# Optimization experiments

Hardware: AMD Instinct MI355X
Metric: run time of the kernel (lower is better)

## Reference

```python
import jax, jax.numpy as jnp
import numpy as np

N_FFT = 512
HOP = 128
WIN = 512
LENGTH = 600  # hardcoded in the original forward


def _hann(n):
    # torch.hann_window default is periodic: 0.5*(1-cos(2*pi*i/n))
    i = jnp.arange(n, dtype=jnp.float32)
    return 0.5 * (1.0 - jnp.cos(2.0 * jnp.pi * i / n))


def setup_inputs() -> dict:
    key = jax.random.key(0)
    x = jax.random.normal(key, (8192, 1, 257, 6, 2), dtype=jnp.float32)
    return {"x": x}


def reference(x):
    B, C, F, T, D = x.shape  # C==1, F==n_fft//2+1, D==2
    # view(B, F, T, D) + view_as_complex
    spec = x[:, 0, :, :, 0] + 1j * x[:, 0, :, :, 1]          # [B, F, T] complex64
    # inverse real FFT per frame (torch.istft, normalized=False, onesided=True)
    frames = jnp.fft.irfft(spec.transpose(0, 2, 1), n=N_FFT, axis=-1)  # [B, T, n_fft]
    win = _hann(WIN)                                          # [n_fft] (win_length == n_fft)
    frames = frames * win                                     # synthesis windowing
    # overlap-add
    L = HOP * (T - 1) + N_FFT
    idx = jnp.arange(T)[:, None] * HOP + jnp.arange(N_FFT)[None, :]  # [T, n_fft]
    y = jnp.zeros((B, L), dtype=frames.dtype).at[:, idx].add(frames)  # [B, L]
    # window-square envelope normalization (COLA division)
    env = jnp.zeros((L,), dtype=frames.dtype).at[idx].add(win * win)  # [L]
    # center=True trim of n_fft//2, then length=600 crop
    start = N_FFT // 2
    sig = y[:, start:start + LENGTH] / env[start:start + LENGTH]       # [B, 600]
    return sig[:, None, :]                                    # unsqueeze(1) -> [B, 1, 600]
```

## Files before the change

kernel.cpp:

```cpp
#include <hip/hip_runtime.h>
#include <hip/hip_bf16.h>


#define NFFT   512
#define HOP    128
#define KDIM   3084
#define KP     3104
#define NOUT   600
#define NP     640
#define BM     64
#define BN     128
#define BK     32
#define KSTEPS (KP / BK)
#define LDA    40

typedef short s16x8 __attribute__((ext_vector_type(8)));
typedef float f32x4 __attribute__((ext_vector_type(4)));

static __device__ __forceinline__ unsigned short bf16_bits(float f) {
    __hip_bfloat16 b = __float2bfloat16(f);
    return *(unsigned short*)&b;
}

__global__ __launch_bounds__(256) void gen_W(unsigned short* __restrict__ Wt) {
    __shared__ float costab[512];
    __shared__ __align__(16) unsigned short rowbuf[KP];
    const int l   = blockIdx.x;
    const int tid = threadIdx.x;
    const float w0 = 6.283185307179586f / 512.0f;

    *(int4*)(rowbuf + tid * 8) = make_int4(0, 0, 0, 0);
    if (tid < 132) *(int4*)(rowbuf + (256 + tid) * 8) = make_int4(0, 0, 0, 0);
    costab[tid]       = __cosf((float)tid * w0);
    costab[tid + 256] = __cosf((float)(tid + 256) * w0);
    __syncthreads();

    if (l < NOUT) {
        const int p = l + 256;
        float env = 0.0f;
#pragma unroll
        for (int tt = 0; tt < 6; ++tt) {
            int m = p - HOP * tt;
            if (m >= 0 && m < NFFT) {
                float w = 0.5f - 0.5f * costab[m];
                env += w * w;
            }
        }
        const float inv = 1.0f / (512.0f * env);
        for (int f = tid; f <= 256; f += 256) {
            float cf = (f == 0 || f == 256) ? 1.0f : 2.0f;
#pragma unroll
            for (int t = 0; t < 6; ++t) {
                int n = p - HOP * t;
                if (n >= 0 && n < NFFT) {
                    float w = 0.5f - 0.5f * costab[n];
                    float scale = cf * w * inv;
                    int a = (f * n) & 511;
                    float c = costab[a];
                    float s = costab[(a + 384) & 511];
                    rowbuf[f * 12 + t * 2 + 0] = bf16_bits(scale * c);
                    rowbuf[f * 12 + t * 2 + 1] = bf16_bits(-scale * s);
                }
            }
        }
    }
    __syncthreads();

    unsigned short* dst = Wt + (size_t)l * KP;
    *(int4*)(dst + tid * 8) = *(const int4*)(rowbuf + tid * 8);
    if (tid < 132) *(int4*)(dst + (256 + tid) * 8) = *(const int4*)(rowbuf + (256 + tid) * 8);
}

__global__ __launch_bounds__(256, 4) void gemm_kernel(
        const float* __restrict__ X,
        const unsigned short* __restrict__ Wt,
        float* __restrict__ out) {
    __shared__ __align__(16) unsigned short As[BM * LDA];
    __shared__ __align__(16) unsigned short Bs[BN * LDA];

    const int tid = threadIdx.x;
    const int bid = blockIdx.x;
    const int xcd = bid & 7;
    const int idx = bid >> 3;
    const int mt  = xcd * 16 + idx / 5;
    const int nt  = idx % 5;
    const int mBase = mt * BM;
    const int nBase = nt * BN;

    const int lane = tid & 63;
    const int wave = tid >> 6;
    const int wm   = (wave & 1) * 32;
    const int wn   = (wave >> 1) * 64;
    const int lrow = lane & 15;
    const int quad = lane >> 4;
    const int koff = quad * 8;

    f32x4 acc[2][4];
#pragma unroll
    for (int i = 0; i < 2; ++i)
#pragma unroll
        for (int j = 0; j < 4; ++j) acc[i][j] = (f32x4){0.f, 0.f, 0.f, 0.f};

    for (int step = 0; step < KSTEPS; ++step) {
        const int k0 = step * BK;
#pragma unroll
        for (int pass = 0; pass < 2; ++pass) {
            int unit = pass * 256 + tid;
            int row  = unit >> 3;
            int u    = unit & 7;
            int gcol = k0 + u * 4;
            float4 v = make_float4(0.f, 0.f, 0.f, 0.f);
            if (gcol < KDIM)
                v = *(const float4*)(X + (size_t)(mBase + row) * KDIM + gcol);
            unsigned long long pk = (unsigned long long)bf16_bits(v.x) |
                                    ((unsigned long long)bf16_bits(v.y) << 16) |
                                    ((unsigned long long)bf16_bits(v.z) << 32) |
                                    ((unsigned long long)bf16_bits(v.w) << 48);
            *(unsigned long long*)(As + row * LDA + u * 4) = pk;
        }
#pragma unroll
        for (int pass = 0; pass < 2; ++pass) {
            int unit = pass * 256 + tid;
            int row  = unit >> 2;
            int u    = unit & 3;
            int gcol = k0 + u * 8;
            s16x8 v = *(const s16x8*)(const void*)(Wt + (size_t)(nBase + row) * KP + gcol);
            *(s16x8*)(void*)(Bs + row * LDA + u * 8) = v;
        }
        __syncthreads();

        s16x8 bfr[4];
#pragma unroll
        for (int j = 0; j < 4; ++j)
            bfr[j] = *(const s16x8*)(const void*)(Bs + (wn + j * 16 + lrow) * LDA + koff);
#pragma unroll
        for (int i = 0; i < 2; ++i) {
            s16x8 afr = *(const s16x8*)(const void*)(As + (wm + i * 16 + lrow) * LDA + koff);
#pragma unroll
            for (int j = 0; j < 4; ++j)
                acc[i][j] = __builtin_amdgcn_mfma_f32_16x16x32_bf16(
                    afr, bfr[j], acc[i][j], 0, 0, 0);
        }
        __syncthreads();
    }

#pragma unroll
    for (int i = 0; i < 2; ++i) {
#pragma unroll
        for (int j = 0; j < 4; ++j) {
            int gn = nBase + wn + j * 16 + lrow;
            if (gn < NOUT) {
#pragma unroll
                for (int r = 0; r < 4; ++r) {
                    int gm = mBase + wm + i * 16 + quad * 4 + r;
                    out[(size_t)gm * NOUT + gn] = acc[i][j][r];
                }
            }
        }
    }
}

extern "C" void kernel_launch(void* const* d_in, const int* in_sizes, int n_in,
                              void* d_out, int out_size, void* d_ws, size_t ws_size,
                              hipStream_t stream) {
    const float* X = (const float*)d_in[0];
    unsigned short* W = (unsigned short*)d_ws;
    float* out = (float*)d_out;

    gen_W<<<dim3(NP), 256, 0, stream>>>(W);
    gemm_kernel<<<dim3(128 * 5), 256, 0, stream>>>(X, W, out);
}
```

Measured before the change: 255.7 us.

## Split-K GEMM in two halves with atomic accumulation and register prefetch

Splits the K dimension into two halves so the grid doubles to 1280 blocks, and combines partial results with atomicAdd into an output zeroed by a memset. It also prefetches the next K-step's global loads into registers while the current step's MFMAs run, and raises the launch-bounds occupancy hint from 4 to 5. The aim is better CU occupancy and hiding of global-load latency, at the cost of an extra memset, doubled output traffic through atomics, and nondeterministic float summation order.

```diff
diff --git a/kernel.cpp b/kernel.cpp
--- a/kernel.cpp
+++ b/kernel.cpp
@@ -71,7 +71,7 @@
     if (tid < 132) *(int4*)(dst + (256 + tid) * 8) = *(const int4*)(rowbuf + (256 + tid) * 8);
 }
 
-__global__ __launch_bounds__(256, 4) void gemm_kernel(
+__global__ __launch_bounds__(256, 5) void gemm_kernel(
         const float* __restrict__ X,
         const unsigned short* __restrict__ Wt,
         float* __restrict__ out) {
@@ -79,13 +79,17 @@
     __shared__ __align__(16) unsigned short Bs[BN * LDA];
 
     const int tid = threadIdx.x;
-    const int bid = blockIdx.x;
-    const int xcd = bid & 7;
-    const int idx = bid >> 3;
-    const int mt  = xcd * 16 + idx / 5;
-    const int nt  = idx % 5;
+    const int bid  = blockIdx.x;
+    const int xcd  = bid & 7;
+    const int rest = bid >> 3;
+    const int mt   = xcd * 16 + rest / 10;
+    const int sub  = rest % 10;
+    const int nt   = sub >> 1;
+    const int kidx = sub & 1;
     const int mBase = mt * BM;
     const int nBase = nt * BN;
+    const int sBeg  = kidx ? 49 : 0;
+    const int sEnd  = kidx ? KSTEPS : 49;
 
     const int lane = tid & 63;
     const int wave = tid >> 6;
@@ -95,39 +99,59 @@
     const int quad = lane >> 4;
     const int koff = quad * 8;
 
+    const int aRow0 = tid >> 3,  aU0 = tid & 7;
+    const int aRow1 = (256 + tid) >> 3, aU1 = tid & 7;
+    const int bRow0 = tid >> 2,  bU0 = tid & 3;
+    const int bRow1 = (256 + tid) >> 2, bU1 = tid & 3;
+
     f32x4 acc[2][4];
 #pragma unroll
     for (int i = 0; i < 2; ++i)
 #pragma unroll
         for (int j = 0; j < 4; ++j) acc[i][j] = (f32x4){0.f, 0.f, 0.f, 0.f};
 
-    for (int step = 0; step < KSTEPS; ++step) {
-        const int k0 = step * BK;
+    float4 av[2];
+    s16x8  bv[2];
+    {
+        const int k0 = sBeg * BK;
+        int g0 = k0 + aU0 * 4;
+        av[0] = make_float4(0.f, 0.f, 0.f, 0.f);
+        av[1] = make_float4(0.f, 0.f, 0.f, 0.f);
+        if (g0 < KDIM) {
+            av[0] = *(const float4*)(X + (size_t)(mBase + aRow0) * KDIM + g0);
+            av[1] = *(const float4*)(X + (size_t)(mBase + aRow1) * KDIM + g0);
+        }
+        bv[0] = *(const s16x8*)(const void*)(Wt + (size_t)(nBase + bRow0) * KP + k0 + bU0 * 8);
+        bv[1] = *(const s16x8*)(const void*)(Wt + (size_t)(nBase + bRow1) * KP + k0 + bU1 * 8);
+    }
+
+    for (int step = sBeg; step < sEnd; ++step) {
 #pragma unroll
-        for (int pass = 0; pass < 2; ++pass) {
-            int unit = pass * 256 + tid;
-            int row  = unit >> 3;
-            int u    = unit & 7;
-            int gcol = k0 + u * 4;
-            float4 v = make_float4(0.f, 0.f, 0.f, 0.f);
-            if (gcol < KDIM)
-                v = *(const float4*)(X + (size_t)(mBase + row) * KDIM + gcol);
+        for (int p = 0; p < 2; ++p) {
+            float4 v = av[p];
             unsigned long long pk = (unsigned long long)bf16_bits(v.x) |
                                     ((unsigned long long)bf16_bits(v.y) << 16) |
                                     ((unsigned long long)bf16_bits(v.z) << 32) |
                                     ((unsigned long long)bf16_bits(v.w) << 48);
-            *(unsigned long long*)(As + row * LDA + u * 4) = pk;
+            int row = p ? aRow1 : aRow0;
+            *(unsigned long long*)(As + row * LDA + aU0 * 4) = pk;
         }
-#pragma unroll
-        for (int pass = 0; pass < 2; ++pass) {
-            int unit = pass * 256 + tid;
-            int row  = unit >> 2;
-            int u    = unit & 3;
-            int gcol = k0 + u * 8;
-            s16x8 v = *(const s16x8*)(const void*)(Wt + (size_t)(nBase + row) * KP + gcol);
-            *(s16x8*)(void*)(Bs + row * LDA + u * 8) = v;
+        *(s16x8*)(void*)(Bs + bRow0 * LDA + bU0 * 8) = bv[0];
+        *(s16x8*)(void*)(Bs + bRow1 * LDA + bU1 * 8) = bv[1];
+        __syncthreads();
+
+        if (step + 1 < sEnd) {
+            const int k0 = (step + 1) * BK;
+            int g0 = k0 + aU0 * 4;
+            av[0] = make_float4(0.f, 0.f, 0.f, 0.f);
+            av[1] = make_float4(0.f, 0.f, 0.f, 0.f);
+            if (g0 < KDIM) {
+                av[0] = *(const float4*)(X + (size_t)(mBase + aRow0) * KDIM + g0);
+                av[1] = *(const float4*)(X + (size_t)(mBase + aRow1) * KDIM + g0);
+            }
+            bv[0] = *(const s16x8*)(const void*)(Wt + (size_t)(nBase + bRow0) * KP + k0 + bU0 * 8);
+            bv[1] = *(const s16x8*)(const void*)(Wt + (size_t)(nBase + bRow1) * KP + k0 + bU1 * 8);
         }
-        __syncthreads();
 
         s16x8 bfr[4];
 #pragma unroll
@@ -153,7 +177,7 @@
 #pragma unroll
                 for (int r = 0; r < 4; ++r) {
                     int gm = mBase + wm + i * 16 + quad * 4 + r;
-                    out[(size_t)gm * NOUT + gn] = acc[i][j][r];
+                    atomicAdd(out + (size_t)gm * NOUT + gn, acc[i][j][r]);
                 }
             }
         }
@@ -167,6 +191,7 @@
     unsigned short* W = (unsigned short*)d_ws;
     float* out = (float*)d_out;
 
+    hipMemsetAsync(d_out, 0, (size_t)out_size * sizeof(float), stream);
     gen_W<<<dim3(NP), 256, 0, stream>>>(W);
-    gemm_kernel<<<dim3(128 * 5), 256, 0, stream>>>(X, W, out);
+    gemm_kernel<<<dim3(128 * 5 * 2), 256, 0, stream>>>(X, W, out);
 }
```

Measured after the change: 256.4 us. No clear change (+0.3%).

## Drop LDS staging, load MFMA fragments directly, split-K by two with atomics

Applied to the files above, without the earlier changes.

Removes the shared-memory tiles and barriers from the GEMM. Each lane now reads its A fragment straight from global fp32 and converts it to bf16 in registers, and reads B from a pre-swizzled panel layout of W written by gen_W. The K dimension is split into two halves across twice as many blocks, with partial sums combined through atomicAdd into an output that is zeroed by a memset first. This aims to cut synchronization overhead and raise parallelism. The cost is redundant global loads, since each fragment is no longer shared through LDS, plus atomic traffic and an extra memset.

```diff
diff --git a/kernel.cpp b/kernel.cpp
--- a/kernel.cpp
+++ b/kernel.cpp
@@ -6,13 +6,11 @@
 #define HOP    128
 #define KDIM   3084
 #define KP     3104
+#define NPAN   (KP / 8)
 #define NOUT   600
 #define NP     640
 #define BM     64
 #define BN     128
-#define BK     32
-#define KSTEPS (KP / BK)
-#define LDA    40
 
 typedef short s16x8 __attribute__((ext_vector_type(8)));
 typedef float f32x4 __attribute__((ext_vector_type(4)));
@@ -22,7 +20,16 @@
     return *(unsigned short*)&b;
 }
 
-__global__ __launch_bounds__(256) void gen_W(unsigned short* __restrict__ Wt) {
+static __device__ __forceinline__ s16x8 cvt8(float4 v0, float4 v1) {
+    s16x8 r;
+    r[0] = (short)bf16_bits(v0.x); r[1] = (short)bf16_bits(v0.y);
+    r[2] = (short)bf16_bits(v0.z); r[3] = (short)bf16_bits(v0.w);
+    r[4] = (short)bf16_bits(v1.x); r[5] = (short)bf16_bits(v1.y);
+    r[6] = (short)bf16_bits(v1.z); r[7] = (short)bf16_bits(v1.w);
+    return r;
+}
+
+__global__ __launch_bounds__(256) void gen_W(unsigned short* __restrict__ W2) {
     __shared__ float costab[512];
     __shared__ __align__(16) unsigned short rowbuf[KP];
     const int l   = blockIdx.x;
@@ -30,7 +37,7 @@
     const float w0 = 6.283185307179586f / 512.0f;
 
     *(int4*)(rowbuf + tid * 8) = make_int4(0, 0, 0, 0);
-    if (tid < 132) *(int4*)(rowbuf + (256 + tid) * 8) = make_int4(0, 0, 0, 0);
+    if (tid < NPAN - 256) *(int4*)(rowbuf + (256 + tid) * 8) = make_int4(0, 0, 0, 0);
     costab[tid]       = __cosf((float)tid * w0);
     costab[tid + 256] = __cosf((float)(tid + 256) * w0);
     __syncthreads();
@@ -66,24 +73,22 @@
     }
     __syncthreads();
 
-    unsigned short* dst = Wt + (size_t)l * KP;
-    *(int4*)(dst + tid * 8) = *(const int4*)(rowbuf + tid * 8);
-    if (tid < 132) *(int4*)(dst + (256 + tid) * 8) = *(const int4*)(rowbuf + (256 + tid) * 8);
+    for (int c = tid; c < NPAN; c += 256)
+        *(int4*)(W2 + ((size_t)c * NP + l) * 8) = *(const int4*)(rowbuf + c * 8);
 }
 
 __global__ __launch_bounds__(256, 4) void gemm_kernel(
         const float* __restrict__ X,
-        const unsigned short* __restrict__ Wt,
+        const unsigned short* __restrict__ W2,
         float* __restrict__ out) {
-    __shared__ __align__(16) unsigned short As[BM * LDA];
-    __shared__ __align__(16) unsigned short Bs[BN * LDA];
-
     const int tid = threadIdx.x;
-    const int bid = blockIdx.x;
-    const int xcd = bid & 7;
-    const int idx = bid >> 3;
-    const int mt  = xcd * 16 + idx / 5;
-    const int nt  = idx % 5;
+    const int bid  = blockIdx.x;
+    const int xcd  = bid & 7;
+    const int rest = bid >> 3;
+    const int mt   = xcd * 16 + rest / 10;
+    const int sub  = rest % 10;
+    const int nt   = sub >> 1;
+    const int kidx = sub & 1;
     const int mBase = mt * BM;
     const int nBase = nt * BN;
 
@@ -93,7 +98,14 @@
     const int wn   = (wave >> 1) * 64;
     const int lrow = lane & 15;
     const int quad = lane >> 4;
-    const int koff = quad * 8;
+
+    const int sBeg = kidx ? 48 : 0;
+    const int sEnd = kidx ? 96 : 48;
+
+    const float* aP0 = X + (size_t)(mBase + wm + lrow) * KDIM + quad * 8;
+    const float* aP1 = aP0 + (size_t)16 * KDIM;
+    const unsigned short* bP =
+        W2 + ((size_t)(sBeg * 4 + quad) * NP + (nBase + wn + lrow)) * 8;
 
     f32x4 acc[2][4];
 #pragma unroll
@@ -101,47 +113,43 @@
 #pragma unroll
         for (int j = 0; j < 4; ++j) acc[i][j] = (f32x4){0.f, 0.f, 0.f, 0.f};
 
-    for (int step = 0; step < KSTEPS; ++step) {
-        const int k0 = step * BK;
-#pragma unroll
-        for (int pass = 0; pass < 2; ++pass) {
-            int unit = pass * 256 + tid;
-            int row  = unit >> 3;
-            int u    = unit & 7;
-            int gcol = k0 + u * 4;
-            float4 v = make_float4(0.f, 0.f, 0.f, 0.f);
-            if (gcol < KDIM)
-                v = *(const float4*)(X + (size_t)(mBase + row) * KDIM + gcol);
-            unsigned long long pk = (unsigned long long)bf16_bits(v.x) |
-                                    ((unsigned long long)bf16_bits(v.y) << 16) |
-                                    ((unsigned long long)bf16_bits(v.z) << 32) |
-                                    ((unsigned long long)bf16_bits(v.w) << 48);
-            *(unsigned long long*)(As + row * LDA + u * 4) = pk;
-        }
-#pragma unroll
-        for (int pass = 0; pass < 2; ++pass) {
-            int unit = pass * 256 + tid;
-            int row  = unit >> 2;
-            int u    = unit & 3;
-            int gcol = k0 + u * 8;
-            s16x8 v = *(const s16x8*)(const void*)(Wt + (size_t)(nBase + row) * KP + gcol);
-            *(s16x8*)(void*)(Bs + row * LDA + u * 8) = v;
-        }
-        __syncthreads();
-
+#pragma unroll 2
+    for (int step = sBeg; step < sEnd; ++step) {
         s16x8 bfr[4];
 #pragma unroll
         for (int j = 0; j < 4; ++j)
-            bfr[j] = *(const s16x8*)(const void*)(Bs + (wn + j * 16 + lrow) * LDA + koff);
+            bfr[j] = *(const s16x8*)(const void*)(bP + j * 128);
 #pragma unroll
         for (int i = 0; i < 2; ++i) {
-            s16x8 afr = *(const s16x8*)(const void*)(As + (wm + i * 16 + lrow) * LDA + koff);
+            const float* ap = (i ? aP1 : aP0) + step * 32;
+            float4 v0 = *(const float4*)(ap);
+            float4 v1 = *(const float4*)(ap + 4);
+            s16x8 afr = cvt8(v0, v1);
 #pragma unroll
             for (int j = 0; j < 4; ++j)
                 acc[i][j] = __builtin_amdgcn_mfma_f32_16x16x32_bf16(
                     afr, bfr[j], acc[i][j], 0, 0, 0);
         }
-        __syncthreads();
+        bP += (size_t)4 * NP * 8;
+    }
+
+    if (kidx) {
+        s16x8 bfr[4];
+#pragma unroll
+        for (int j = 0; j < 4; ++j)
+            bfr[j] = *(const s16x8*)(const void*)(bP + j * 128);
+        const float4 z4 = make_float4(0.f, 0.f, 0.f, 0.f);
+#pragma unroll
+        for (int i = 0; i < 2; ++i) {
+            const float* ap = (i ? aP1 : aP0) + 96 * 32;
+            float4 v0 = (quad < 2) ? *(const float4*)(ap)     : z4;
+            float4 v1 = (quad < 1) ? *(const float4*)(ap + 4) : z4;
+            s16x8 afr = cvt8(v0, v1);
+#pragma unroll
+            for (int j = 0; j < 4; ++j)
+                acc[i][j] = __builtin_amdgcn_mfma_f32_16x16x32_bf16(
+                    afr, bfr[j], acc[i][j], 0, 0, 0);
+        }
     }
 
 #pragma unroll
@@ -153,7 +161,7 @@
 #pragma unroll
                 for (int r = 0; r < 4; ++r) {
                     int gm = mBase + wm + i * 16 + quad * 4 + r;
-                    out[(size_t)gm * NOUT + gn] = acc[i][j][r];
+                    atomicAdd(out + (size_t)gm * NOUT + gn, acc[i][j][r]);
                 }
             }
         }
@@ -164,9 +172,10 @@
                               void* d_out, int out_size, void* d_ws, size_t ws_size,
                               hipStream_t stream) {
     const float* X = (const float*)d_in[0];
-    unsigned short* W = (unsigned short*)d_ws;
+    unsigned short* W2 = (unsigned short*)d_ws;
     float* out = (float*)d_out;
 
-    gen_W<<<dim3(NP), 256, 0, stream>>>(W);
-    gemm_kernel<<<dim3(128 * 5), 256, 0, stream>>>(X, W, out);
+    hipMemsetAsync(d_out, 0, (size_t)out_size * sizeof(float), stream);
+    gen_W<<<dim3(NP), 256, 0, stream>>>(W2);
+    gemm_kernel<<<dim3(128 * 5 * 2), 256, 0, stream>>>(X, W2, out);
 }
```

Result: slower. 293.9 us (+14.9%).
